# Kernel optimization log

Measured on AMD Instinct MI355X. Metric: run time of the kernel, lower is better.

The kernel has to match this reference:

```python
import jax, jax.numpy as jnp
import numpy as np

B, L = 8, 2048          # images, lines per image
C_IN, HW = 256, 128     # backbone feature channels, spatial size
DIM_LOI = 128
N_PTS0, N_PTS1 = 32, 8  # sampled points per line, after maxpool
SCALE = N_PTS0 // N_PTS1
EPS = 1e-5


def setup_inputs() -> dict:
    key = jax.random.key(0)
    ks = jax.random.split(key, 24)
    d = {}
    d['feature'] = jax.random.normal(ks[0], (B, C_IN, HW, HW), jnp.float32)
    # line endpoints in pixel coords [0, 128)
    d['lines'] = jax.random.uniform(ks[1], (B, L, 2, 2), jnp.float32) * HW
    # fc1: 1x1 conv 256 -> 128
    d['fc1_w'] = jax.random.normal(ks[2], (DIM_LOI, C_IN), jnp.float32) * 0.05
    d['fc1_b'] = jnp.zeros((DIM_LOI,), jnp.float32)
    planes = DIM_LOI // 2
    def bn(k, c):
        k1, k2, k3 = jax.random.split(k, 3)
        return (jax.random.normal(k1, (c,), jnp.float32) * 0.1 + 1.0,
                jax.random.normal(k2, (c,), jnp.float32) * 0.1,
                jax.random.normal(k3, (c,), jnp.float32) * 0.05,
                jax.random.uniform(jax.random.fold_in(k, 7), (c,), jnp.float32, 0.5, 1.5))
    d['bn1_g'], d['bn1_b'], d['bn1_m'], d['bn1_v'] = bn(ks[3], DIM_LOI)
    d['conv1_w'] = jax.random.normal(ks[4], (planes, DIM_LOI), jnp.float32) * 0.05
    d['conv1_b'] = jnp.zeros((planes,), jnp.float32)
    d['bn2_g'], d['bn2_b'], d['bn2_m'], d['bn2_v'] = bn(ks[5], planes)
    d['conv2_w'] = jax.random.normal(ks[6], (planes, planes, 3), jnp.float32) * 0.05
    d['conv2_b'] = jnp.zeros((planes,), jnp.float32)
    d['bn3_g'], d['bn3_b'], d['bn3_m'], d['bn3_v'] = bn(ks[7], planes)
    d['conv3_w'] = jax.random.normal(ks[8], (DIM_LOI, planes), jnp.float32) * 0.05
    d['conv3_b'] = jnp.zeros((DIM_LOI,), jnp.float32)
    d['fc2_w'] = jax.random.normal(ks[9], (1, DIM_LOI * N_PTS1), jnp.float32) * 0.02
    d['fc2_b'] = jnp.zeros((1,), jnp.float32)
    return d


def _bn(x, g, b, m, v):
    # x: [N, C, T], eval-mode batchnorm
    s = g * jax.lax.rsqrt(v + EPS)
    return x * s[None, :, None] + (b - m * s)[None, :, None]


def _loi_forward(feature, lines, fc1_w, fc1_b,
                 bn1_g, bn1_b, bn1_m, bn1_v, conv1_w, conv1_b,
                 bn2_g, bn2_b, bn2_m, bn2_v, conv2_w, conv2_b,
                 bn3_g, bn3_b, bn3_m, bn3_v, conv3_w, conv3_b,
                 fc2_w, fc2_b):
    # fc1: 1x1 conv -> [B, DIM_LOI, H, W]
    x = jnp.einsum('oc,bchw->bohw', fc1_w, feature) + fc1_b[None, :, None, None]

    # sample N_PTS0 points per line: p = p0*lam + p1*(1-lam) - 0.5
    lam = jnp.linspace(0.0, 1.0, N_PTS0, dtype=lines.dtype)  # [P]
    pts = (lines[:, :, 0, None, :] * lam[None, None, :, None]
           + lines[:, :, 1, None, :] * (1.0 - lam[None, None, :, None]) - 0.5)  # [B,L,P,2]
    px, py = pts[..., 0], pts[..., 1]
    px0 = jnp.clip(jnp.floor(px), 0.0, HW - 1.0)
    py0 = jnp.clip(jnp.floor(py), 0.0, HW - 1.0)
    px1 = jnp.clip(px0 + 1.0, 0.0, HW - 1.0)
    py1 = jnp.clip(py0 + 1.0, 0.0, HW - 1.0)
    px0l, py0l = px0.astype(jnp.int32), py0.astype(jnp.int32)
    px1l, py1l = px1.astype(jnp.int32), py1.astype(jnp.int32)

    def gather(f, ix, iy):  # f: [C,H,W], ix/iy: [L,P] -> [C,L,P]
        return f[:, ix, iy]

    gat = jax.vmap(gather)  # over batch
    xp = (gat(x, px0l, py0l) * ((px1 - px) * (py1 - py))[:, None]
          + gat(x, px1l, py0l) * ((px - px0) * (py1 - py))[:, None]
          + gat(x, px0l, py1l) * ((px1 - px) * (py - py0))[:, None]
          + gat(x, px1l, py1l) * ((px - px0) * (py - py0))[:, None])  # [B,C,L,P]

    xp = xp.transpose(0, 2, 1, 3).reshape(B * L, DIM_LOI, N_PTS0)  # [N,C,P]
    # MaxPool1d(kernel=stride=SCALE)
    xp = xp.reshape(B * L, DIM_LOI, N_PTS1, SCALE).max(axis=-1)  # [N,C,T=8]

    # Bottleneck1D residual: x + op(x)
    h = jax.nn.relu(_bn(xp, bn1_g, bn1_b, bn1_m, bn1_v))
    h = jnp.einsum('oc,nct->not', conv1_w, h) + conv1_b[None, :, None]
    h = jax.nn.relu(_bn(h, bn2_g, bn2_b, bn2_m, bn2_v))
    h = jax.lax.conv_general_dilated(h, conv2_w, (1,), [(1, 1)],
                                     dimension_numbers=('NCH', 'OIH', 'NCH'))
    h = h + conv2_b[None, :, None]
    h = jax.nn.relu(_bn(h, bn3_g, bn3_b, bn3_m, bn3_v))
    h = jnp.einsum('oc,nct->not', conv3_w, h) + conv3_b[None, :, None]
    xp = xp + h

    # fc2: ReLU -> Linear(dim_loi*n_pts1, 1)
    flat = jax.nn.relu(xp).reshape(B * L, DIM_LOI * N_PTS1)
    logits = (flat @ fc2_w.T + fc2_b).reshape(-1)  # [B*L]
    return logits


def reference(feature, lines, fc1_w, fc1_b,
              bn1_g, bn1_b, bn1_m, bn1_v, conv1_w, conv1_b,
              bn2_g, bn2_b, bn2_m, bn2_v, conv2_w, conv2_b,
              bn3_g, bn3_b, bn3_m, bn3_v, conv3_w, conv3_b,
              fc2_w, fc2_b):
    return _loi_forward(feature, lines, fc1_w, fc1_b,
                        bn1_g, bn1_b, bn1_m, bn1_v, conv1_w, conv1_b,
                        bn2_g, bn2_b, bn2_m, bn2_v, conv2_w, conv2_b,
                        bn3_g, bn3_b, bn3_m, bn3_v, conv3_w, conv3_b,
                        fc2_w, fc2_b)
```

## Files before the change

kernel.cpp:

```cpp
#include <hip/hip_runtime.h>

#define EPSBN 1e-5f

typedef _Float16 f16;
typedef _Float16 f16x8 __attribute__((ext_vector_type(8)));
typedef _Float16 f16x4 __attribute__((ext_vector_type(4)));
typedef _Float16 f16x2 __attribute__((ext_vector_type(2)));
typedef float    f32x4 __attribute__((ext_vector_type(4)));

__device__ inline unsigned int pack2(float a, float b) {
    union { f16x2 h; unsigned int u; } cv;
    cv.h[0] = (f16)a; cv.h[1] = (f16)b;
    return cv.u;
}
__device__ inline f16x8 hmax8(f16x8 a, f16x8 b) {
    f16x8 r;
    #pragma unroll
    for (int i = 0; i < 8; ++i) r[i] = a[i] > b[i] ? a[i] : b[i];
    return r;
}
__device__ inline f16x8 relu8(f16x8 v) {
    f16x8 r;
    #pragma unroll
    for (int i = 0; i < 8; ++i) r[i] = v[i] > (f16)0.f ? v[i] : (f16)0.f;
    return r;
}

__global__ void wprep_kernel(const float* __restrict__ fc1w,
                             const float* __restrict__ w1,
                             const float* __restrict__ w2,
                             const float* __restrict__ w3,
                             f16* __restrict__ dst) {
    const int i = blockIdx.x * 256 + threadIdx.x;
    float v;
    if (i < 32768)      v = fc1w[i];
    else if (i < 40960) v = w1[i - 32768];
    else if (i < 53248) {
        const int j = i - 40960, tau = j >> 12, rest = j & 4095;
        v = w2[rest * 3 + tau];
    } else              v = w3[i - 53248];
    dst[i] = (f16)v;
}

__global__ __launch_bounds__(512, 4)
void fc1_mfma(const float* __restrict__ feat,
              const f16*   __restrict__ w16,
              const float* __restrict__ bias,
              f16*         __restrict__ xmap) {
    __shared__ union {
        float fbuf[2][8368];
        f16   epi[256][136];
    } u;

    const int tid  = threadIdx.x;
    const int wv   = tid >> 6, lane = tid & 63;
    const int n16  = lane & 15, quad = lane >> 4;
    const int img  = blockIdx.x & 7;
    const int p0   = (blockIdx.x >> 3) << 8;

    const float* fimg = feat + (((size_t)img) << 22);

    f32x4 acc[8][2];
    #pragma unroll
    for (int ot = 0; ot < 8; ++ot) {
        acc[ot][0] = (f32x4){0.f, 0.f, 0.f, 0.f};
        acc[ot][1] = (f32x4){0.f, 0.f, 0.f, 0.f};
    }

    auto issue = [&](int s, int b) {
        #pragma unroll
        for (int i = 0; i < 4; ++i) {
            const int cl = wv * 4 + i;
            const int ch = s * 32 + cl;
            const float* src = fimg + (((size_t)ch) << 14) + p0 + lane * 4;
            float* dst = &u.fbuf[b][cl * 260 + (cl >> 3) * 16];
            __builtin_amdgcn_global_load_lds(
                (const __attribute__((address_space(1))) void*)src,
                (__attribute__((address_space(3))) void*)dst, 16, 0, 0);
        }
    };

    issue(0, 0);
    __syncthreads();

    for (int s = 0; s < 8; ++s) {
        const int cur = s & 1;
        if (s < 7) issue(s + 1, cur ^ 1);

        f16x8 xf[2];
        #pragma unroll
        for (int pt = 0; pt < 2; ++pt) {
            const int pbase = wv * 32 + pt * 16 + n16;
            const float* fb = &u.fbuf[cur][quad * 16 + pbase];
            f16x8 xv;
            #pragma unroll
            for (int j = 0; j < 8; ++j)
                xv[j] = (f16)fb[(quad * 8 + j) * 260];
            xf[pt] = xv;
        }

        const f16* wrow = w16 + (size_t)n16 * 256 + s * 32 + quad * 8;
        #pragma unroll
        for (int ot = 0; ot < 8; ++ot) {
            const f16x8 wf = *(const f16x8*)(wrow + ot * 4096);
            acc[ot][0] = __builtin_amdgcn_mfma_f32_16x16x32_f16(wf, xf[0], acc[ot][0], 0, 0, 0);
            acc[ot][1] = __builtin_amdgcn_mfma_f32_16x16x32_f16(wf, xf[1], acc[ot][1], 0, 0, 0);
        }
        __syncthreads();
    }

    #pragma unroll
    for (int ot = 0; ot < 8; ++ot) {
        const float4 bq = *(const float4*)&bias[ot * 16 + quad * 4];
        const float bqa[4] = {bq.x, bq.y, bq.z, bq.w};
        #pragma unroll
        for (int pt = 0; pt < 2; ++pt) {
            f16x4 h;
            #pragma unroll
            for (int r = 0; r < 4; ++r) h[r] = (f16)(acc[ot][pt][r] + bqa[r]);
            *(f16x4*)&u.epi[wv * 32 + pt * 16 + n16][ot * 16 + quad * 4] = h;
        }
    }
    __syncthreads();

    #pragma unroll
    for (int it = 0; it < 8; ++it) {
        const int idx = it * 512 + tid;
        const int row = idx >> 4, seg = idx & 15;
        const float4 v = *(const float4*)&u.epi[row][seg * 8];
        *(float4*)&xmap[(((size_t)(img * 16384 + p0 + row)) << 7) + seg * 8] = v;
    }
}

__global__ __launch_bounds__(256)
void loi_kernel(const f16*   __restrict__ x,
                const float* __restrict__ lines,
                const f16*   __restrict__ wsp,
                const float* __restrict__ bn1g, const float* __restrict__ bn1b,
                const float* __restrict__ bn1m, const float* __restrict__ bn1v,
                const float* __restrict__ b1,
                const float* __restrict__ bn2g, const float* __restrict__ bn2b,
                const float* __restrict__ bn2m, const float* __restrict__ bn2v,
                const float* __restrict__ b2,
                const float* __restrict__ bn3g, const float* __restrict__ bn3b,
                const float* __restrict__ bn3m, const float* __restrict__ bn3v,
                const float* __restrict__ b3,
                const float* __restrict__ fc2w, const float* __restrict__ fc2b,
                float* __restrict__ out) {
    __shared__ f16 xp[64][136];
    __shared__ alignas(16) union {
        struct { int toff[256][4]; f16 twgt[256][4]; } tp;
        struct { f16 h1[80][72]; f16 h2[64][72]; } cv;
    } u;
    __shared__ f16 s1h[128], t1h[128];
    __shared__ float s2f[64], t2f[64], s3f[64], t3f[64], b1f[64], b2f[64];
    __shared__ float b3f[128];
    __shared__ float wsum[4][8];

    const f16* w1f16 = wsp + 32768;
    const f16* w2f16 = wsp + 40960;
    const f16* w3f16 = wsp + 53248;

    const int tid  = threadIdx.x;
    const int wv   = tid >> 6, lane = tid & 63;
    const int n16  = lane & 15, quad = lane >> 4;
    const int img  = blockIdx.x & 7;
    const int mblk = blockIdx.x >> 3;

    if (tid < 128) {
        const float s = bn1g[tid] * rsqrtf(bn1v[tid] + EPSBN);
        s1h[tid] = (f16)s; t1h[tid] = (f16)(bn1b[tid] - bn1m[tid] * s);
    }
    if (tid < 64) {
        const float s = bn2g[tid] * rsqrtf(bn2v[tid] + EPSBN);
        s2f[tid] = s; t2f[tid] = bn2b[tid] - bn2m[tid] * s;
        b1f[tid] = b1[tid];
    } else if (tid < 128) {
        const int c = tid - 64;
        const float s = bn3g[c] * rsqrtf(bn3v[c] + EPSBN);
        s3f[c] = s; t3f[c] = bn3b[c] - bn3m[c] * s;
        b2f[c] = b2[c];
    } else {
        b3f[tid - 128] = b3[tid - 128];
    }

    {
        const int li = tid >> 5, pt = tid & 31;
        const int gl = img * 2048 + mblk * 8 + li;
        const float4 ln = *(const float4*)&lines[gl * 4];
        const float lam = (float)pt * (1.0f / 31.0f);
        const float px = ln.x * lam + ln.z * (1.f - lam) - 0.5f;
        const float py = ln.y * lam + ln.w * (1.f - lam) - 0.5f;
        const float px0 = fminf(fmaxf(floorf(px), 0.f), 127.f);
        const float py0 = fminf(fmaxf(floorf(py), 0.f), 127.f);
        const float px1 = fminf(px0 + 1.f, 127.f);
        const float py1 = fminf(py0 + 1.f, 127.f);
        const int ix0 = (int)px0, iy0 = (int)py0;
        const int ix1 = (int)px1, iy1 = (int)py1;
        u.tp.toff[tid][0] = (((ix0 << 7) + iy0) << 7);
        u.tp.toff[tid][1] = (((ix1 << 7) + iy0) << 7);
        u.tp.toff[tid][2] = (((ix0 << 7) + iy1) << 7);
        u.tp.toff[tid][3] = (((ix1 << 7) + iy1) << 7);
        const float wx1 = px1 - px, wx0 = px - px0;
        const float wy1 = py1 - py, wy0 = py - py0;
        u.tp.twgt[tid][0] = (f16)(wx1 * wy1); u.tp.twgt[tid][1] = (f16)(wx0 * wy1);
        u.tp.twgt[tid][2] = (f16)(wx1 * wy0); u.tp.twgt[tid][3] = (f16)(wx0 * wy0);
    }
    __syncthreads();

    {
        const int h  = lane >> 5;
        const int sh = (lane >> 4) & 1;
        const int j  = lane & 15;
        const int li = wv * 2 + h;
        const f16* xbh = x + (((size_t)img) << 21) + 8 * j;
        #pragma unroll
        for (int t = 0; t < 8; ++t) {
            f16x8 m;
            #pragma unroll
            for (int q = 0; q < 8; ++q) m[q] = (f16)(-60000.f);
            #pragma unroll
            for (int ss = 0; ss < 2; ++ss) {
                const int combo = li * 32 + t * 4 + sh * 2 + ss;
                const int4  off = *(const int4*)&u.tp.toff[combo][0];
                const f16x4 tw  = *(const f16x4*)&u.tp.twgt[combo][0];
                const f16x8 g00 = *(const f16x8*)(xbh + off.x);
                const f16x8 g10 = *(const f16x8*)(xbh + off.y);
                const f16x8 g01 = *(const f16x8*)(xbh + off.z);
                const f16x8 g11 = *(const f16x8*)(xbh + off.w);
                f16x8 w0, w1v, w2v, w3v;
                #pragma unroll
                for (int q = 0; q < 8; ++q) {
                    w0[q] = tw[0]; w1v[q] = tw[1]; w2v[q] = tw[2]; w3v[q] = tw[3];
                }
                const f16x8 v = g00 * w0 + g10 * w1v + g01 * w2v + g11 * w3v;
                m = hmax8(m, v);
            }
            union { f16x8 v8; int i4[4]; } cv;
            cv.v8 = m;
            #pragma unroll
            for (int q = 0; q < 4; ++q) cv.i4[q] = __shfl_xor(cv.i4[q], 16, 64);
            m = hmax8(m, cv.v8);
            if (sh == 0) *(f16x8*)&xp[li * 8 + t][8 * j] = m;
        }
    }
    __syncthreads();

    {
        const int r = tid >> 4, seg = tid & 15;
        const int row = (r >> 1) * 10 + (r & 1) * 9;
        *(unsigned long long*)&u.cv.h1[row][seg * 4] = 0ull;
    }

    {
        const int o_lane = wv * 16 + n16;
        f32x4 acc1[4];
        #pragma unroll
        for (int nt = 0; nt < 4; ++nt) acc1[nt] = (f32x4){0.f, 0.f, 0.f, 0.f};
        #pragma unroll
        for (int ks = 0; ks < 4; ++ks) {
            const int k = ks * 32 + quad * 8;
            const f16x8 a  = *(const f16x8*)&w1f16[o_lane * 128 + k];
            const f16x8 s8 = *(const f16x8*)&s1h[k];
            const f16x8 t8 = *(const f16x8*)&t1h[k];
            #pragma unroll
            for (int nt = 0; nt < 4; ++nt) {
                const f16x8 raw = *(const f16x8*)&xp[nt * 16 + n16][k];
                const f16x8 bf = relu8(raw * s8 + t8);
                acc1[nt] = __builtin_amdgcn_mfma_f32_16x16x32_f16(a, bf, acc1[nt], 0, 0, 0);
            }
        }
        #pragma unroll
        for (int nt = 0; nt < 4; ++nt) {
            const int n = nt * 16 + n16;
            const int nprow = (n >> 3) * 10 + (n & 7) + 1;
            #pragma unroll
            for (int r = 0; r < 4; ++r) {
                const int o = wv * 16 + quad * 4 + r;
                const float v = fmaxf((acc1[nt][r] + b1f[o]) * s2f[o] + t2f[o], 0.f);
                u.cv.h1[nprow][o] = (f16)v;
            }
        }
    }
    __syncthreads();

    {
        const int o_lane = wv * 16 + n16;
        f32x4 acc2[4];
        #pragma unroll
        for (int nt = 0; nt < 4; ++nt) acc2[nt] = (f32x4){0.f, 0.f, 0.f, 0.f};
        #pragma unroll
        for (int d = 0; d < 3; ++d) {
            const f16* A2 = w2f16 + d * 4096;
            #pragma unroll
            for (int ks = 0; ks < 2; ++ks) {
                const int k = ks * 32 + quad * 8;
                const f16x8 a = *(const f16x8*)&A2[o_lane * 64 + k];
                #pragma unroll
                for (int nt = 0; nt < 4; ++nt) {
                    const int n = nt * 16 + n16;
                    const int row = (n >> 3) * 10 + (n & 7) + d;
                    const f16x8 bf = *(const f16x8*)&u.cv.h1[row][k];
                    acc2[nt] = __builtin_amdgcn_mfma_f32_16x16x32_f16(a, bf, acc2[nt], 0, 0, 0);
                }
            }
        }
        #pragma unroll
        for (int nt = 0; nt < 4; ++nt) {
            const int n = nt * 16 + n16;
            #pragma unroll
            for (int r = 0; r < 4; ++r) {
                const int o = wv * 16 + quad * 4 + r;
                const float v = fmaxf((acc2[nt][r] + b2f[o]) * s3f[o] + t3f[o], 0.f);
                u.cv.h2[n][o] = (f16)v;
            }
        }
    }
    __syncthreads();

    {
        const int col = n16 & 7, obase = wv * 16 + quad * 4;
        float fcv[2][4];
        #pragma unroll
        for (int h = 0; h < 2; ++h)
            #pragma unroll
            for (int r = 0; r < 4; ++r)
                fcv[h][r] = fc2w[(h * 64 + obase + r) * 8 + col];

        f32x4 acc3[2][4];
        #pragma unroll
        for (int h = 0; h < 2; ++h)
            #pragma unroll
            for (int nt = 0; nt < 4; ++nt) acc3[h][nt] = (f32x4){0.f, 0.f, 0.f, 0.f};
        #pragma unroll
        for (int ks = 0; ks < 2; ++ks) {
            const int k = ks * 32 + quad * 8;
            const f16x8 a0 = *(const f16x8*)&w3f16[(wv * 16 + n16) * 64 + k];
            const f16x8 a1 = *(const f16x8*)&w3f16[(64 + wv * 16 + n16) * 64 + k];
            #pragma unroll
            for (int nt = 0; nt < 4; ++nt) {
                const f16x8 bf = *(const f16x8*)&u.cv.h2[nt * 16 + n16][k];
                acc3[0][nt] = __builtin_amdgcn_mfma_f32_16x16x32_f16(a0, bf, acc3[0][nt], 0, 0, 0);
                acc3[1][nt] = __builtin_amdgcn_mfma_f32_16x16x32_f16(a1, bf, acc3[1][nt], 0, 0, 0);
            }
        }
        float part[4] = {0.f, 0.f, 0.f, 0.f};
        #pragma unroll
        for (int h = 0; h < 2; ++h) {
            const float4 bq = *(const float4*)&b3f[h * 64 + obase];
            const float bqa[4] = {bq.x, bq.y, bq.z, bq.w};
            #pragma unroll
            for (int nt = 0; nt < 4; ++nt) {
                const int n = nt * 16 + n16;
                const f16x4 rx = *(const f16x4*)&xp[n][h * 64 + obase];
                float p = 0.f;
                #pragma unroll
                for (int r = 0; r < 4; ++r) {
                    float v = acc3[h][nt][r] + bqa[r] + (float)rx[r];
                    v = fmaxf(v, 0.f);
                    p += v * fcv[h][r];
                }
                part[nt] += p;
            }
        }
        #pragma unroll
        for (int off_i = 0; off_i < 5; ++off_i) {
            const int off = (int[]){1, 2, 4, 16, 32}[off_i];
            part[0] += __shfl_xor(part[0], off, 64);
            part[1] += __shfl_xor(part[1], off, 64);
            part[2] += __shfl_xor(part[2], off, 64);
            part[3] += __shfl_xor(part[3], off, 64);
        }
        if ((lane & 55) == 0) {
            const int par = (lane >> 3) & 1;
            wsum[wv][0 + par] = part[0];
            wsum[wv][2 + par] = part[1];
            wsum[wv][4 + par] = part[2];
            wsum[wv][6 + par] = part[3];
        }
    }
    __syncthreads();

    if (tid < 8) {
        const float s = wsum[0][tid] + wsum[1][tid] + wsum[2][tid] + wsum[3][tid];
        out[img * 2048 + mblk * 8 + tid] = s + fc2b[0];
    }
}

extern "C" void kernel_launch(void* const* d_in, const int* in_sizes, int n_in,
                              void* d_out, int out_size, void* d_ws, size_t ws_size,
                              hipStream_t stream) {
    const float* feature = (const float*)d_in[0];
    const float* lines   = (const float*)d_in[1];
    const float* fc1_w   = (const float*)d_in[2];
    const float* fc1_b   = (const float*)d_in[3];
    const float* bn1g    = (const float*)d_in[4];
    const float* bn1b    = (const float*)d_in[5];
    const float* bn1m    = (const float*)d_in[6];
    const float* bn1v    = (const float*)d_in[7];
    const float* w1      = (const float*)d_in[8];
    const float* b1      = (const float*)d_in[9];
    const float* bn2g    = (const float*)d_in[10];
    const float* bn2b    = (const float*)d_in[11];
    const float* bn2m    = (const float*)d_in[12];
    const float* bn2v    = (const float*)d_in[13];
    const float* w2      = (const float*)d_in[14];
    const float* b2      = (const float*)d_in[15];
    const float* bn3g    = (const float*)d_in[16];
    const float* bn3b    = (const float*)d_in[17];
    const float* bn3m    = (const float*)d_in[18];
    const float* bn3v    = (const float*)d_in[19];
    const float* w3      = (const float*)d_in[20];
    const float* b3      = (const float*)d_in[21];
    const float* fc2w    = (const float*)d_in[22];
    const float* fc2b    = (const float*)d_in[23];

    f16* xmap = (f16*)d_ws;
    f16* wsp  = (f16*)((char*)d_ws + (size_t)32 * 1024 * 1024);

    wprep_kernel<<<240, 256, 0, stream>>>(fc1_w, w1, w2, w3, wsp);
    fc1_mfma<<<512, 512, 0, stream>>>(feature, wsp, fc1_b, xmap);
    loi_kernel<<<2048, 256, 0, stream>>>(xmap, lines, wsp,
                                         bn1g, bn1b, bn1m, bn1v, b1,
                                         bn2g, bn2b, bn2m, bn2v, b2,
                                         bn3g, bn3b, bn3m, bn3v, b3,
                                         fc2w, fc2b, (float*)d_out);
}
```

Baseline: 285.6 us.

## Restructure fc1 GEMM with 1024-thread blocks, LDS weight staging, 4-deep ring

The fc1 1x1-conv kernel now runs 16 waves per block, split across point groups and output halves. Weights are pre-swizzled into MFMA fragment order and staged in LDS with async global-to-LDS loads. Feature channels stream through a four-slot ring with explicit vmcnt waits and swizzled addressing, so loads overlap the MFMA work. This is meant to hide the memory latency of reading the feature map and to cut redundant global weight loads, at the cost of more LDS per block and a split, two-pass epilogue.

```diff
diff --git a/kernel.cpp b/kernel.cpp
--- a/kernel.cpp
+++ b/kernel.cpp
@@ -8,11 +8,9 @@
 typedef _Float16 f16x2 __attribute__((ext_vector_type(2)));
 typedef float    f32x4 __attribute__((ext_vector_type(4)));
 
-__device__ inline unsigned int pack2(float a, float b) {
-    union { f16x2 h; unsigned int u; } cv;
-    cv.h[0] = (f16)a; cv.h[1] = (f16)b;
-    return cv.u;
-}
+#define AS1 __attribute__((address_space(1)))
+#define AS3 __attribute__((address_space(3)))
+
 __device__ inline f16x8 hmax8(f16x8 a, f16x8 b) {
     f16x8 r;
     #pragma unroll
@@ -33,7 +31,11 @@
                              f16* __restrict__ dst) {
     const int i = blockIdx.x * 256 + threadIdx.x;
     float v;
-    if (i < 32768)      v = fc1w[i];
+    if (i < 32768) {
+        const int k8 = i & 7, otg = (i >> 3) & 7, l = (i >> 6) & 63, s = i >> 12;
+        const int n16l = l & 15, quadl = l >> 4;
+        v = fc1w[(otg * 16 + n16l) * 256 + s * 32 + quadl * 8 + k8];
+    }
     else if (i < 40960) v = w1[i - 32768];
     else if (i < 53248) {
         const int j = i - 40960, tau = j >> 12, rest = j & 4095;
@@ -42,93 +44,120 @@
     dst[i] = (f16)v;
 }
 
-__global__ __launch_bounds__(512, 4)
+__global__ __launch_bounds__(1024, 4)
 void fc1_mfma(const float* __restrict__ feat,
-              const f16*   __restrict__ w16,
+              const f16*   __restrict__ wfrag,
               const float* __restrict__ bias,
               f16*         __restrict__ xmap) {
+    __shared__ f16 wlds[32768];
     __shared__ union {
-        float fbuf[2][8368];
-        f16   epi[256][136];
+        float ring[4][4096];
+        f16   epi[128][136];
     } u;
 
     const int tid  = threadIdx.x;
-    const int wv   = tid >> 6, lane = tid & 63;
+    const int wv   = tid >> 6;
+    const int lane = tid & 63;
     const int n16  = lane & 15, quad = lane >> 4;
+    const int pw   = wv >> 1;
+    const int ow   = wv & 1;
     const int img  = blockIdx.x & 7;
     const int p0   = (blockIdx.x >> 3) << 8;
 
     const float* fimg = feat + (((size_t)img) << 22);
 
-    f32x4 acc[8][2];
-    #pragma unroll
-    for (int ot = 0; ot < 8; ++ot) {
-        acc[ot][0] = (f32x4){0.f, 0.f, 0.f, 0.f};
-        acc[ot][1] = (f32x4){0.f, 0.f, 0.f, 0.f};
-    }
-
-    auto issue = [&](int s, int b) {
-        #pragma unroll
-        for (int i = 0; i < 4; ++i) {
-            const int cl = wv * 4 + i;
-            const int ch = s * 32 + cl;
-            const float* src = fimg + (((size_t)ch) << 14) + p0 + lane * 4;
-            float* dst = &u.fbuf[b][cl * 260 + (cl >> 3) * 16];
-            __builtin_amdgcn_global_load_lds(
-                (const __attribute__((address_space(1))) void*)src,
-                (__attribute__((address_space(3))) void*)dst, 16, 0, 0);
-        }
+    f32x4 acc[2][4];
+    #pragma unroll
+    for (int ptg = 0; ptg < 2; ++ptg)
+        #pragma unroll
+        for (int t = 0; t < 4; ++t) acc[ptg][t] = (f32x4){0.f, 0.f, 0.f, 0.f};
+
+    const int swz = (wv >> 3) << 2;
+    auto issue_hs = [&](int h) {
+        const int ch = h * 16 + wv;
+        const float* src = fimg + (((size_t)ch) << 14) + p0 + ((lane ^ swz) << 2);
+        float* dst = u.ring[h & 3] + (wv << 8);
+        __builtin_amdgcn_global_load_lds((const AS1 void*)src,
+                                         (AS3 void*)dst, 16, 0, 0);
     };
 
-    issue(0, 0);
-    __syncthreads();
-
+    #pragma unroll
+    for (int c4 = 0; c4 < 4; ++c4) {
+        const int c = wv + 16 * c4;
+        __builtin_amdgcn_global_load_lds((const AS1 void*)(wfrag + c * 512 + lane * 8),
+                                         (AS3 void*)(wlds + c * 512), 16, 0, 0);
+    }
+    #pragma unroll
+    for (int h = 0; h < 4; ++h) issue_hs(h);
+
+    const int xswz = (quad & 1) << 2;
+
+    #pragma unroll
     for (int s = 0; s < 8; ++s) {
-        const int cur = s & 1;
-        if (s < 7) issue(s + 1, cur ^ 1);
+        if (s < 7) asm volatile("s_waitcnt vmcnt(2)" ::: "memory");
+        else       asm volatile("s_waitcnt vmcnt(0)" ::: "memory");
+        __builtin_amdgcn_s_barrier();
+        __builtin_amdgcn_sched_barrier(0);
+
+        f16x8 wf[4];
+        #pragma unroll
+        for (int t = 0; t < 4; ++t)
+            wf[t] = *(const f16x8*)&wlds[((s * 64 + lane) * 8 + ow * 4 + t) * 8];
 
         f16x8 xf[2];
         #pragma unroll
-        for (int pt = 0; pt < 2; ++pt) {
-            const int pbase = wv * 32 + pt * 16 + n16;
-            const float* fb = &u.fbuf[cur][quad * 16 + pbase];
+        for (int ptg = 0; ptg < 2; ++ptg) {
+            const int pt   = pw * 32 + ptg * 16 + n16;
+            const int col  = ((((pt >> 2) ^ xswz) << 2) | (pt & 3));
+            const float* fb = u.ring[(2 * s + (quad >> 1)) & 3]
+                              + ((quad & 1) << 11) + col;
             f16x8 xv;
             #pragma unroll
-            for (int j = 0; j < 8; ++j)
-                xv[j] = (f16)fb[(quad * 8 + j) * 260];
-            xf[pt] = xv;
-        }
-
-        const f16* wrow = w16 + (size_t)n16 * 256 + s * 32 + quad * 8;
-        #pragma unroll
-        for (int ot = 0; ot < 8; ++ot) {
-            const f16x8 wf = *(const f16x8*)(wrow + ot * 4096);
-            acc[ot][0] = __builtin_amdgcn_mfma_f32_16x16x32_f16(wf, xf[0], acc[ot][0], 0, 0, 0);
-            acc[ot][1] = __builtin_amdgcn_mfma_f32_16x16x32_f16(wf, xf[1], acc[ot][1], 0, 0, 0);
-        }
+            for (int j = 0; j < 8; ++j) xv[j] = (f16)fb[j << 8];
+            xf[ptg] = xv;
+        }
+
+        #pragma unroll
+        for (int ptg = 0; ptg < 2; ++ptg)
+            #pragma unroll
+            for (int t = 0; t < 4; ++t)
+                acc[ptg][t] = __builtin_amdgcn_mfma_f32_16x16x32_f16(wf[t], xf[ptg],
+                                                                     acc[ptg][t], 0, 0, 0);
+
+        __builtin_amdgcn_sched_barrier(0);
+        __builtin_amdgcn_s_barrier();
+        __builtin_amdgcn_sched_barrier(0);
+        if (s < 6) { issue_hs(2 * s + 4); issue_hs(2 * s + 5); }
+    }
+
+    #pragma unroll
+    for (int P = 0; P < 2; ++P) {
         __syncthreads();
-    }
-
-    #pragma unroll
-    for (int ot = 0; ot < 8; ++ot) {
-        const float4 bq = *(const float4*)&bias[ot * 16 + quad * 4];
-        const float bqa[4] = {bq.x, bq.y, bq.z, bq.w};
-        #pragma unroll
-        for (int pt = 0; pt < 2; ++pt) {
-            f16x4 h;
-            #pragma unroll
-            for (int r = 0; r < 4; ++r) h[r] = (f16)(acc[ot][pt][r] + bqa[r]);
-            *(f16x4*)&u.epi[wv * 32 + pt * 16 + n16][ot * 16 + quad * 4] = h;
-        }
-    }
-    __syncthreads();
-
-    #pragma unroll
-    for (int it = 0; it < 8; ++it) {
-        const int idx = it * 512 + tid;
-        const int row = idx >> 4, seg = idx & 15;
-        const float4 v = *(const float4*)&u.epi[row][seg * 8];
-        *(float4*)&xmap[(((size_t)(img * 16384 + p0 + row)) << 7) + seg * 8] = v;
+        if ((pw >> 2) == P) {
+            #pragma unroll
+            for (int ptg = 0; ptg < 2; ++ptg) {
+                const int rowl = (pw & 3) * 32 + ptg * 16 + n16;
+                #pragma unroll
+                for (int t = 0; t < 4; ++t) {
+                    const int o = ow * 64 + t * 16 + quad * 4;
+                    const float4 bq = *(const float4*)&bias[o];
+                    f16x4 hv;
+                    hv[0] = (f16)(acc[ptg][t][0] + bq.x);
+                    hv[1] = (f16)(acc[ptg][t][1] + bq.y);
+                    hv[2] = (f16)(acc[ptg][t][2] + bq.z);
+                    hv[3] = (f16)(acc[ptg][t][3] + bq.w);
+                    *(f16x4*)&u.epi[rowl][o] = hv;
+                }
+            }
+        }
+        __syncthreads();
+        #pragma unroll
+        for (int it = 0; it < 2; ++it) {
+            const int idx = it * 1024 + tid;
+            const int rowl = idx >> 4, seg = idx & 15;
+            const float4 v = *(const float4*)&u.epi[rowl][seg * 8];
+            *(float4*)&xmap[(((size_t)(img * 16384 + p0 + P * 128 + rowl)) << 7) + seg * 8] = v;
+        }
     }
 }
 
@@ -419,7 +448,7 @@
     f16* wsp  = (f16*)((char*)d_ws + (size_t)32 * 1024 * 1024);
 
     wprep_kernel<<<240, 256, 0, stream>>>(fc1_w, w1, w2, w3, wsp);
-    fc1_mfma<<<512, 512, 0, stream>>>(feature, wsp, fc1_b, xmap);
+    fc1_mfma<<<512, 1024, 0, stream>>>(feature, wsp, fc1_b, xmap);
     loi_kernel<<<2048, 256, 0, stream>>>(xmap, lines, wsp,
                                          bn1g, bn1b, bn1m, bn1v, b1,
                                          bn2g, bn2b, bn2m, bn2v, b2,
```

Result: no change. 281.9 us (-1.3%).
